# Kernel optimization log

Measured on AMD Instinct MI355X. Metric: run time of the kernel, lower is better.

## Reference

```python
import jax, jax.numpy as jnp
import numpy as np

N_NODES = 50000
N_EDGES = 800000
B, S, D = 512, 200, 128
H = 8


def setup_inputs() -> dict:
    key = jax.random.key(0)
    ks = iter(jax.random.split(key, 64))
    def nrm(shape, scale=0.05):
        return jax.random.normal(next(ks), shape, dtype=jnp.float32) * scale
    inp = {
        'hist_seq': jax.random.randint(next(ks), (B, S), 0, N_NODES, dtype=jnp.int32),
        'hist_answers': jax.random.randint(next(ks), (B, S), 0, 2, dtype=jnp.int32),
        'new_seq': jax.random.randint(next(ks), (B, S), 0, N_NODES, dtype=jnp.int32),
        'edge_index': jax.random.randint(next(ks), (2, N_EDGES), 0, N_NODES, dtype=jnp.int32),
        'node_x': nrm((N_NODES, D)),
        'gcn_w0': nrm((D, D)), 'gcn_b0': jnp.zeros((D,), jnp.float32),
        'gcn_w1': nrm((D, D)), 'gcn_b1': jnp.zeros((D,), jnp.float32),
        'gcn_w2': nrm((D, D)), 'gcn_b2': jnp.zeros((D,), jnp.float32),
        'ln0_g': jnp.ones((D,), jnp.float32), 'ln0_b': jnp.zeros((D,), jnp.float32),
        'ln1_g': jnp.ones((D,), jnp.float32), 'ln1_b': jnp.zeros((D,), jnp.float32),
        'ln2_g': jnp.ones((D,), jnp.float32), 'ln2_b': jnp.zeros((D,), jnp.float32),
        'ln3_g': jnp.ones((D,), jnp.float32), 'ln3_b': jnp.zeros((D,), jnp.float32),
        'corr_emb': nrm((2, D)),
        'lin0_w': nrm((2 * D, D)), 'lin0_b': jnp.zeros((D,), jnp.float32),
        'lin1_w': nrm((D, D)), 'lin2_w': nrm((D, D)), 'lin3_w': nrm((D, D)),
        'lin4_w': nrm((D, 1)), 'lin4_b': jnp.zeros((1,), jnp.float32),
        'pos_emb': nrm((S, D)),
        'mha_wq': nrm((D, D)), 'mha_bq': jnp.zeros((D,), jnp.float32),
        'mha_wk': nrm((D, D)), 'mha_bk': jnp.zeros((D,), jnp.float32),
        'mha_wv': nrm((D, D)), 'mha_bv': jnp.zeros((D,), jnp.float32),
        'mha_wo': nrm((D, D)), 'mha_bo': jnp.zeros((D,), jnp.float32),
        'ffn0_w': nrm((D, D)), 'ffn0_b': jnp.zeros((D,), jnp.float32),
        'ffn1_w': nrm((D, D)), 'ffn1_b': jnp.zeros((D,), jnp.float32),
    }
    return inp


def _layer_norm(x, g, b, eps=1e-5):
    m = jnp.mean(x, axis=-1, keepdims=True)
    v = jnp.var(x, axis=-1, keepdims=True)
    return (x - m) * jax.lax.rsqrt(v + eps) * g + b


def _forward(hist_seq, hist_answers, new_seq, edge_index, node_x,
             gcn_w0, gcn_b0, gcn_w1, gcn_b1, gcn_w2, gcn_b2,
             ln0_g, ln0_b, ln1_g, ln1_b, ln2_g, ln2_b, ln3_g, ln3_b,
             corr_emb, lin0_w, lin0_b, lin1_w, lin2_w, lin3_w, lin4_w, lin4_b,
             pos_emb, mha_wq, mha_bq, mha_wk, mha_bk, mha_wv, mha_bv,
             mha_wo, mha_bo, ffn0_w, ffn0_b, ffn1_w, ffn1_b):
    N = node_x.shape[0]
    loop = jnp.arange(N, dtype=edge_index.dtype)
    src = jnp.concatenate([edge_index[0], loop])  # self-loops as in PyG GCNConv
    dst = jnp.concatenate([edge_index[1], loop])
    deg = jax.ops.segment_sum(jnp.ones_like(dst, dtype=node_x.dtype), dst, num_segments=N)
    dis = jax.lax.rsqrt(deg)  # deg >= 1 (self-loops)
    norm = dis[src] * dis[dst]

    def gcn(x, W, b):
        xw = x @ W
        return jax.ops.segment_sum(norm[:, None] * xw[src], dst, num_segments=N) + b

    x = _layer_norm(jax.nn.relu(gcn(node_x, gcn_w0, gcn_b0)), ln0_g, ln0_b)
    x = _layer_norm(jax.nn.relu(gcn(x, gcn_w1, gcn_b1)), ln1_g, ln1_b)
    x = jax.nn.relu(gcn(x, gcn_w2, gcn_b2))  # last GCN layer: no LN

    # vectorized embedding gathers (the original's per-element loops)
    hist_emb = x[hist_seq]            # [B,S,D]
    new_emb = x[new_seq]              # [B,S,D]
    ans_emb = corr_emb[hist_answers]  # [B,S,D]

    inter = jnp.concatenate([hist_emb, ans_emb], axis=-1) @ lin0_w + lin0_b
    inter = inter + pos_emb[None]  # [B,S,D]

    v = inter @ lin1_w
    k = inter @ lin2_w
    q = new_emb @ lin3_w

    b_, s_, d_ = q.shape
    dh = d_ // H
    qh = (q @ mha_wq + mha_bq).reshape(b_, s_, H, dh)
    kh = (k @ mha_wk + mha_bk).reshape(b_, s_, H, dh)
    vh = (v @ mha_wv + mha_bv).reshape(b_, s_, H, dh)
    scores = jnp.einsum('bqhd,bkhd->bhqk', qh, kh) / jnp.sqrt(jnp.asarray(dh, q.dtype))
    causal = jnp.triu(jnp.ones((s_, s_), dtype=bool), k=1)
    scores = jnp.where(causal[None, None], -jnp.inf, scores)
    attn = jax.nn.softmax(scores, axis=-1)
    ao = jnp.einsum('bhqk,bkhd->bqhd', attn, vh).reshape(b_, s_, d_)
    ao = ao @ mha_wo + mha_bo

    atn = _layer_norm(ao + q, ln2_g, ln2_b)
    ffn = jax.nn.relu(atn @ ffn0_w + ffn0_b) @ ffn1_w + ffn1_b
    out = _layer_norm(ffn + atn, ln3_g, ln3_b)
    pred = (out @ lin4_w + lin4_b)[..., 0]  # squeeze -> [B,S]
    return pred


def reference(hist_seq, hist_answers, new_seq, edge_index, node_x,
              gcn_w0, gcn_b0, gcn_w1, gcn_b1, gcn_w2, gcn_b2,
              ln0_g, ln0_b, ln1_g, ln1_b, ln2_g, ln2_b, ln3_g, ln3_b,
              corr_emb, lin0_w, lin0_b, lin1_w, lin2_w, lin3_w, lin4_w, lin4_b,
              pos_emb, mha_wq, mha_bq, mha_wk, mha_bk, mha_wv, mha_bv,
              mha_wo, mha_bo, ffn0_w, ffn0_b, ffn1_w, ffn1_b):
    return _forward(hist_seq, hist_answers, new_seq, edge_index, node_x,
                    gcn_w0, gcn_b0, gcn_w1, gcn_b1, gcn_w2, gcn_b2,
                    ln0_g, ln0_b, ln1_g, ln1_b, ln2_g, ln2_b, ln3_g, ln3_b,
                    corr_emb, lin0_w, lin0_b, lin1_w, lin2_w, lin3_w, lin4_w, lin4_b,
                    pos_emb, mha_wq, mha_bq, mha_wk, mha_bk, mha_wv, mha_bv,
                    mha_wo, mha_bo, ffn0_w, ffn0_b, ffn1_w, ffn1_b)
```

## Files before the change

### kernel.cpp

```cpp
#include <hip/hip_runtime.h>
#include <math.h>

#define N_NODES 50000
#define N_EDGES 800000
#define B_ 512
#define S_ 200
#define D_ 128
#define BS_ (B_*S_)
#define PSTR 228

typedef unsigned short u16;
typedef unsigned int u32;
using bfrag = __attribute__((ext_vector_type(8))) short;
using f32x4 = __attribute__((ext_vector_type(4))) float;

__device__ __forceinline__ u16 f2bf(float f) {
  return (u16)((__float_as_uint(f) + 0x8000u) >> 16);
}
__device__ __forceinline__ float bf2f(u16 v) { return __uint_as_float(((u32)v) << 16); }
__device__ __forceinline__ float bflo(u32 v) { return __uint_as_float(v << 16); }
__device__ __forceinline__ float bfhi(u32 v) { return __uint_as_float(v & 0xffff0000u); }
__device__ __forceinline__ u32 pack2(float a, float b) {
  return (u32)f2bf(a) | ((u32)f2bf(b) << 16);
}
#define MFMA16(a, b, c) __builtin_amdgcn_mfma_f32_16x16x32_bf16((a), (b), (c), 0, 0, 0)

#define STAGE_W(Wsrc) \
  for (int i_ = threadIdx.x; i_ < 2048; i_ += 256) { \
    int c_ = i_ >> 4, kg_ = i_ & 15; \
    *(uint4*)(sW + c_ * 136 + kg_ * 8) = *(const uint4*)((Wsrc) + c_ * 128 + kg_ * 8); \
  }

__global__ void zero_i32_kernel(int* __restrict__ p, int n) {
  int i = blockIdx.x * 256 + threadIdx.x;
  if (i < n) p[i] = 0;
}

__global__ void f2bf8_kernel(const float* __restrict__ in, u16* __restrict__ out, int n8) {
  int i = blockIdx.x * 256 + threadIdx.x;
  if (i >= n8) return;
  float4 a = ((const float4*)in)[i * 2];
  float4 b = ((const float4*)in)[i * 2 + 1];
  uint4 o;
  o.x = pack2(a.x, a.y); o.y = pack2(a.z, a.w);
  o.z = pack2(b.x, b.y); o.w = pack2(b.z, b.w);
  ((uint4*)out)[i] = o;
}

__global__ __launch_bounds__(256) void wprep_kernel(
    const float* __restrict__ gcn_w0, const float* __restrict__ gcn_w1,
    const float* __restrict__ gcn_w2, const float* __restrict__ lin0_w,
    const float* __restrict__ lin3_w, const float* __restrict__ mha_wo,
    const float* __restrict__ ffn0_w, const float* __restrict__ ffn1_w,
    const float* __restrict__ lin1_w, const float* __restrict__ lin2_w,
    const float* __restrict__ mha_wq, const float* __restrict__ mha_wk,
    const float* __restrict__ mha_wv, const float* __restrict__ corr_emb,
    u16* __restrict__ g0T, u16* __restrict__ g1T, u16* __restrict__ g2T,
    u16* __restrict__ l0T, u16* __restrict__ l3T, u16* __restrict__ woT,
    u16* __restrict__ f0T, u16* __restrict__ f1T,
    u16* __restrict__ wqT, u16* __restrict__ wkT, u16* __restrict__ wvT,
    float* __restrict__ c01) {
  int bb = blockIdx.x;
  if (bb < 512) {
    const float* W; u16* D;
    switch (bb >> 6) {
      case 0: W = gcn_w0; D = g0T; break;
      case 1: W = gcn_w1; D = g1T; break;
      case 2: W = gcn_w2; D = g2T; break;
      case 3: W = lin0_w; D = l0T; break;
      case 4: W = lin3_w; D = l3T; break;
      case 5: W = mha_wo; D = woT; break;
      case 6: W = ffn0_w; D = f0T; break;
      default: W = ffn1_w; D = f1T; break;
    }
    int i = (bb & 63) * 256 + threadIdx.x;
    int k = i >> 7, c = i & 127;
    D[c * 128 + k] = f2bf(W[k * 128 + c]);
  } else if (bb < 704) {
    const float* X; const float* Y; u16* D;
    switch ((bb - 512) >> 6) {
      case 0: X = lin3_w; Y = mha_wq; D = wqT; break;
      case 1: X = lin2_w; Y = mha_wk; D = wkT; break;
      default: X = lin1_w; Y = mha_wv; D = wvT; break;
    }
    int i = ((bb - 512) & 63) * 256 + threadIdx.x;
    int k = i >> 7, c = i & 127;
    float acc = 0.f;
    for (int t = 0; t < 128; ++t) acc += X[k * 128 + t] * Y[t * 128 + c];
    D[c * 128 + k] = f2bf(acc);
  } else {
    int idx = threadIdx.x;
    int i = idx >> 7, j = idx & 127;
    float acc = 0.f;
    for (int t = 0; t < 128; ++t)
      acc += corr_emb[i * 128 + t] * lin0_w[128 * 128 + t * 128 + j];
    c01[idx] = acc;
  }
}

__global__ void pc_kernel(const float* __restrict__ lin0_b, const float* __restrict__ pos_emb,
                          const float* __restrict__ c01, float* __restrict__ pc) {
  int i = blockIdx.x * 256 + threadIdx.x;
  int c = i & 127, s = (i >> 7) % S_, a = i / (128 * S_);
  pc[i] = lin0_b[c] + pos_emb[s * 128 + c] + c01[a * 128 + c];
}

__global__ void hist_kernel(const int* __restrict__ dst, int* __restrict__ cnt, int E) {
  int e = blockIdx.x * 256 + threadIdx.x;
  if (e < E) atomicAdd(&cnt[dst[e]], 1);
}

__global__ __launch_bounds__(1024) void scanA_kernel(
    const int* __restrict__ cnt, int* __restrict__ locpref,
    int* __restrict__ btot, float* __restrict__ dis, int N) {
  __shared__ int wsum[16];
  int t = threadIdx.x, lane = t & 63, wid = t >> 6;
  int i = blockIdx.x * 1024 + t;
  int v = (i < N) ? cnt[i] : 0;
  if (i < N) dis[i] = rsqrtf(1.f + (float)v);
  int x = v;
  #pragma unroll
  for (int off = 1; off < 64; off <<= 1) {
    int y = __shfl_up(x, off);
    if (lane >= off) x += y;
  }
  if (lane == 63) wsum[wid] = x;
  __syncthreads();
  if (wid == 0 && lane < 16) {
    int s = wsum[lane];
    #pragma unroll
    for (int off = 1; off < 16; off <<= 1) {
      int y = __shfl_up(s, off);
      if (lane >= off) s += y;
    }
    wsum[lane] = s;
  }
  __syncthreads();
  int woff = (wid > 0) ? wsum[wid - 1] : 0;
  if (i < N) locpref[i] = woff + x - v;
  if (t == 1023) btot[blockIdx.x] = woff + x;
}

__global__ void scanB_kernel(const int* __restrict__ btot, int* __restrict__ boff, int nb) {
  int lane = threadIdx.x;
  int v = (lane < nb) ? btot[lane] : 0;
  int x = v;
  #pragma unroll
  for (int off = 1; off < 64; off <<= 1) {
    int y = __shfl_up(x, off);
    if (lane >= off) x += y;
  }
  if (lane < nb) boff[lane] = x - v;
}

__global__ void scanC_kernel(const int* __restrict__ locpref, const int* __restrict__ boff,
                             int* __restrict__ row_ptr, int* __restrict__ fill, int N) {
  int i = blockIdx.x * 256 + threadIdx.x;
  if (i < N) {
    int r = locpref[i] + boff[i >> 10];
    row_ptr[i] = r; fill[i] = r;
  }
  if (i == 0) row_ptr[N] = N_EDGES;
}

__global__ void scatter_kernel(const int* __restrict__ src, const int* __restrict__ dst,
                               int* __restrict__ fill, int* __restrict__ csr_src, int E) {
  int e = blockIdx.x * 256 + threadIdx.x;
  if (e >= E) return;
  int d = dst[e];
  int pos = atomicAdd(&fill[d], 1);
  csr_src[pos] = src[e];
}

__global__ __launch_bounds__(256) void gemm_bf16_kernel(
    const u16* __restrict__ A, const u16* __restrict__ wT,
    u16* __restrict__ C, int M) {
  __shared__ u16 ldsb[4][16 * 136];
  int t = threadIdx.x;
  int w = t >> 6, l = t & 63, lr = l & 15, lg = l >> 4;
  int r0 = blockIdx.x * 64 + w * 16;

  int row = r0 + lr;
  const u16* Arow = A + (size_t)(row < M ? row : 0) * 128;

  bfrag a[4];
  #pragma unroll
  for (int ks = 0; ks < 4; ++ks) a[ks] = *(const bfrag*)(Arow + ks * 32 + lg * 8);

  f32x4 acc[8];
  #pragma unroll
  for (int ct = 0; ct < 8; ++ct) acc[ct] = (f32x4){0.f, 0.f, 0.f, 0.f};
  #pragma unroll
  for (int ks = 0; ks < 4; ++ks)
    #pragma unroll
    for (int ct = 0; ct < 8; ++ct) {
      bfrag b = *(const bfrag*)(wT + (size_t)(ct * 16 + lr) * 128 + ks * 32 + lg * 8);
      acc[ct] = MFMA16(a[ks], b, acc[ct]);
    }
  #pragma unroll
  for (int ct = 0; ct < 8; ++ct)
    #pragma unroll
    for (int i = 0; i < 4; ++i)
      ldsb[w][(lg * 4 + i) * 136 + ct * 16 + lr] = f2bf(acc[ct][i]);
  #pragma unroll
  for (int j = 0; j < 4; ++j) {
    int c = j * 64 + l;
    int rw = c >> 4, ch = c & 15;
    int r = r0 + rw;
    if (r < M)
      *(uint4*)(C + (size_t)r * 128 + ch * 8) = *(const uint4*)&ldsb[w][rw * 136 + ch * 8];
  }
}

__global__ __launch_bounds__(256) void agg_kernel(
    const u16* __restrict__ xw, const float* __restrict__ dis,
    const int* __restrict__ row_ptr, const int* __restrict__ csr_src,
    const float* __restrict__ bias, const float* __restrict__ lng,
    const float* __restrict__ lnb, u16* __restrict__ out, int N, int doLN) {
  int t = threadIdx.x;
  int n = blockIdx.x * 4 + (t >> 6);
  if (n >= N) return;
  int l = t & 63, cg = l & 15, eg = l >> 4;
  float dn = dis[n];
  float acc[8] = {0.f, 0.f, 0.f, 0.f, 0.f, 0.f, 0.f, 0.f};
  if (eg == 0) {
    uint4 r = *(const uint4*)(xw + (size_t)n * 128 + cg * 8);
    float w = dn * dn;
    acc[0] += w * bflo(r.x); acc[1] += w * bfhi(r.x);
    acc[2] += w * bflo(r.y); acc[3] += w * bfhi(r.y);
    acc[4] += w * bflo(r.z); acc[5] += w * bfhi(r.z);
    acc[6] += w * bflo(r.w); acc[7] += w * bfhi(r.w);
  }
  int e1 = row_ptr[n + 1];
  int e = row_ptr[n] + eg;
  int sn = (e < e1) ? csr_src[e] : -1;
  while (sn >= 0) {
    int s = sn;
    e += 4;
    sn = (e < e1) ? csr_src[e] : -1;
    float w = dis[s] * dn;
    uint4 r = *(const uint4*)(xw + (size_t)s * 128 + cg * 8);
    acc[0] += w * bflo(r.x); acc[1] += w * bfhi(r.x);
    acc[2] += w * bflo(r.y); acc[3] += w * bfhi(r.y);
    acc[4] += w * bflo(r.z); acc[5] += w * bfhi(r.z);
    acc[6] += w * bflo(r.w); acc[7] += w * bfhi(r.w);
  }
  #pragma unroll
  for (int j = 0; j < 8; ++j) {
    acc[j] += __shfl_xor(acc[j], 16);
    acc[j] += __shfl_xor(acc[j], 32);
  }
  int c0 = cg * 8;
  #pragma unroll
  for (int j = 0; j < 8; ++j) acc[j] = fmaxf(acc[j] + bias[c0 + j], 0.f);
  if (doLN) {
    float s1 = 0.f, s2 = 0.f;
    #pragma unroll
    for (int j = 0; j < 8; ++j) { s1 += acc[j]; s2 += acc[j] * acc[j]; }
    #pragma unroll
    for (int off = 1; off < 16; off <<= 1) {
      s1 += __shfl_xor(s1, off);
      s2 += __shfl_xor(s2, off);
    }
    float mean = s1 * (1.f / 128.f);
    float var = s2 * (1.f / 128.f) - mean * mean;
    float inv = rsqrtf(var + 1e-5f);
    #pragma unroll
    for (int j = 0; j < 8; ++j)
      acc[j] = (acc[j] - mean) * inv * lng[c0 + j] + lnb[c0 + j];
  }
  if (eg == 0) {
    uint4 o;
    o.x = pack2(acc[0], acc[1]); o.y = pack2(acc[2], acc[3]);
    o.z = pack2(acc[4], acc[5]); o.w = pack2(acc[6], acc[7]);
    *(uint4*)(out + (size_t)n * 128 + cg * 8) = o;
  }
}

__global__ __launch_bounds__(256) void qkv_kernel(
    const u16* __restrict__ xa, const int* __restrict__ hist,
    const int* __restrict__ ans, const int* __restrict__ nseq,
    const u16* __restrict__ l0T, const float* __restrict__ pc,
    const u16* __restrict__ wkT, const float* __restrict__ bk,
    const u16* __restrict__ wvT, const float* __restrict__ bv,
    const u16* __restrict__ wqT, const float* __restrict__ bq,
    u16* __restrict__ khout, u16* __restrict__ vhout,
    u16* __restrict__ qhout, int nblk) {
  __shared__ u16 sW[128 * 136];
  __shared__ u16 ldsb[4][16 * 136];
  int bb = blockIdx.x;
  int t = threadIdx.x, w = t >> 6, l = t & 63, lr = l & 15, lg = l >> 4;
  f32x4 acc[8];

  if (bb < nblk) {
    int r0 = bb * 64 + w * 16;
    int arow = hist[r0 + lr];
    const u16* Arow = xa + (size_t)arow * 128;
    bfrag a[4];
    #pragma unroll
    for (int ks = 0; ks < 4; ++ks) a[ks] = *(const bfrag*)(Arow + ks * 32 + lg * 8);

    STAGE_W(l0T);
    __syncthreads();
    #pragma unroll
    for (int ct = 0; ct < 8; ++ct) acc[ct] = (f32x4){0.f, 0.f, 0.f, 0.f};
    #pragma unroll
    for (int ks = 0; ks < 4; ++ks)
      #pragma unroll
      for (int ct = 0; ct < 8; ++ct) {
        bfrag b = *(const bfrag*)(sW + (ct * 16 + lr) * 136 + ks * 32 + lg * 8);
        acc[ct] = MFMA16(a[ks], b, acc[ct]);
      }
    int pcoff[4];
    #pragma unroll
    for (int i = 0; i < 4; ++i) {
      int r = r0 + lg * 4 + i;
      pcoff[i] = (ans[r] * S_ + (r % S_)) * 128;
    }
    #pragma unroll
    for (int ct = 0; ct < 8; ++ct) {
      int col = ct * 16 + lr;
      #pragma unroll
      for (int i = 0; i < 4; ++i)
        ldsb[w][(lg * 4 + i) * 136 + col] = f2bf(acc[ct][i] + pc[pcoff[i] + col]);
    }
    bfrag a2[4];
    #pragma unroll
    for (int ks = 0; ks < 4; ++ks)
      a2[ks] = *(const bfrag*)(&ldsb[w][lr * 136 + ks * 32 + lg * 8]);
    __syncthreads();

    STAGE_W(wkT);
    __syncthreads();
    #pragma unroll
    for (int ct = 0; ct < 8; ++ct) acc[ct] = (f32x4){0.f, 0.f, 0.f, 0.f};
    #pragma unroll
    for (int ks = 0; ks < 4; ++ks)
      #pragma unroll
      for (int ct = 0; ct < 8; ++ct) {
        bfrag b = *(const bfrag*)(sW + (ct * 16 + lr) * 136 + ks * 32 + lg * 8);
        acc[ct] = MFMA16(a2[ks], b, acc[ct]);
      }
    #pragma unroll
    for (int ct = 0; ct < 8; ++ct)
      #pragma unroll
      for (int i = 0; i < 4; ++i)
        ldsb[w][(lg * 4 + i) * 136 + ct * 16 + lr] = f2bf(acc[ct][i] + bk[ct * 16 + lr]);
    #pragma unroll
    for (int j = 0; j < 4; ++j) {
      int c = j * 64 + l;
      int head = c >> 5, rw = (c >> 1) & 15, half = c & 1;
      *(uint4*)(khout + ((size_t)head * BS_ + r0 + rw) * 16 + half * 8) =
          *(const uint4*)&ldsb[w][rw * 136 + head * 16 + half * 8];
    }
    __syncthreads();

    STAGE_W(wvT);
    __syncthreads();
    #pragma unroll
    for (int ct = 0; ct < 8; ++ct) acc[ct] = (f32x4){0.f, 0.f, 0.f, 0.f};
    #pragma unroll
    for (int ks = 0; ks < 4; ++ks)
      #pragma unroll
      for (int ct = 0; ct < 8; ++ct) {
        bfrag b = *(const bfrag*)(sW + (ct * 16 + lr) * 136 + ks * 32 + lg * 8);
        acc[ct] = MFMA16(a2[ks], b, acc[ct]);
      }
    #pragma unroll
    for (int ct = 0; ct < 8; ++ct)
      #pragma unroll
      for (int i = 0; i < 4; ++i)
        ldsb[w][(lg * 4 + i) * 136 + ct * 16 + lr] = f2bf(acc[ct][i] + bv[ct * 16 + lr]);
    #pragma unroll
    for (int j = 0; j < 4; ++j) {
      int c = j * 64 + l;
      int head = c >> 5, rw = (c >> 1) & 15, half = c & 1;
      *(uint4*)(vhout + ((size_t)head * BS_ + r0 + rw) * 16 + half * 8) =
          *(const uint4*)&ldsb[w][rw * 136 + head * 16 + half * 8];
    }
  } else {
    int r0 = (bb - nblk) * 64 + w * 16;
    int arow = nseq[r0 + lr];
    const u16* Arow = xa + (size_t)arow * 128;
    bfrag a[4];
    #pragma unroll
    for (int ks = 0; ks < 4; ++ks) a[ks] = *(const bfrag*)(Arow + ks * 32 + lg * 8);

    STAGE_W(wqT);
    __syncthreads();
    #pragma unroll
    for (int ct = 0; ct < 8; ++ct) acc[ct] = (f32x4){0.f, 0.f, 0.f, 0.f};
    #pragma unroll
    for (int ks = 0; ks < 4; ++ks)
      #pragma unroll
      for (int ct = 0; ct < 8; ++ct) {
        bfrag b = *(const bfrag*)(sW + (ct * 16 + lr) * 136 + ks * 32 + lg * 8);
        acc[ct] = MFMA16(a[ks], b, acc[ct]);
      }
    #pragma unroll
    for (int ct = 0; ct < 8; ++ct)
      #pragma unroll
      for (int i = 0; i < 4; ++i)
        ldsb[w][(lg * 4 + i) * 136 + ct * 16 + lr] =
            f2bf((acc[ct][i] + bq[ct * 16 + lr]) * 0.25f);
    #pragma unroll
    for (int j = 0; j < 4; ++j) {
      int c = j * 64 + l;
      int head = c >> 5, rw = (c >> 1) & 15, half = c & 1;
      *(uint4*)(qhout + ((size_t)head * BS_ + r0 + rw) * 16 + half * 8) =
          *(const uint4*)&ldsb[w][rw * 136 + head * 16 + half * 8];
    }
  }
}

__global__ __launch_bounds__(256) void attn_mfma_kernel(
    u16* qh_ao, const u16* __restrict__ kh, const u16* __restrict__ vh) {
  __shared__ u16 Kl[208 * 24];
  __shared__ u16 Vt[16 * 232];
  __shared__ u16 Pl[4 * 16 * PSTR];
  int b = blockIdx.x >> 3, h = blockIdx.x & 7;
  int t = threadIdx.x;
  size_t base = ((size_t)h * BS_ + (size_t)b * S_) * 16;

  for (int i = t; i < 208 * 2; i += 256) {
    int key = i >> 1, d = (i & 1) * 8;
    uint4 v = make_uint4(0, 0, 0, 0);
    if (key < S_) v = *(const uint4*)(kh + base + (size_t)key * 16 + d);
    *(uint4*)(Kl + key * 24 + d) = v;
  }
  for (int i = t; i < 16 * 232; i += 256) {
    int d = i / 232, key = i - d * 232;
    Vt[d * 232 + key] = (key < S_) ? vh[base + (size_t)key * 16 + d] : (u16)0;
  }
  for (int i = t; i < 4 * 16 * PSTR / 2; i += 256) ((u32*)Pl)[i] = 0;
  __syncthreads();

  int w = t >> 6, l = t & 63, lr = l & 15, lg = l >> 4;
  u16* Pw = Pl + w * 16 * PSTR;
  const f32x4 zero4 = {0.f, 0.f, 0.f, 0.f};
  u32 qpack = (w == 0) ? 0xFC71u : (w == 1) ? 0xFB80u : (w == 2) ? 0xFA92u : 0x6543u;
  int qlocal = lg * 4;

  for (int s = 0; s < 4; ++s) {
    int qi = (qpack >> (4 * s)) & 15;
    if (qi == 15) break;
    bfrag aq = (bfrag){0, 0, 0, 0, 0, 0, 0, 0};
    int qrow = qi * 16 + lr;
    if (lg < 2 && qrow < S_)
      aq = *(const bfrag*)(qh_ao + base + (size_t)qrow * 16 + lg * 8);
    float rsum[4] = {0.f, 0.f, 0.f, 0.f};
    for (int kj = 0; kj < qi; ++kj) {
      bfrag bk = (bfrag){0, 0, 0, 0, 0, 0, 0, 0};
      if (lg < 2) bk = *(const bfrag*)(Kl + (kj * 16 + lr) * 24 + lg * 8);
      f32x4 sc = MFMA16(aq, bk, zero4);
      #pragma unroll
      for (int i = 0; i < 4; ++i) {
        float p = __expf(sc[i]);
        rsum[i] += p;
        Pw[(qlocal + i) * PSTR + kj * 16 + lr] = f2bf(p);
      }
    }
    {
      bfrag bk = (bfrag){0, 0, 0, 0, 0, 0, 0, 0};
      if (lg < 2) bk = *(const bfrag*)(Kl + (qi * 16 + lr) * 24 + lg * 8);
      f32x4 sc = MFMA16(aq, bk, zero4);
      #pragma unroll
      for (int i = 0; i < 4; ++i) {
        if (lr <= qlocal + i) {
          float p = __expf(sc[i]);
          rsum[i] += p;
          Pw[(qlocal + i) * PSTR + qi * 16 + lr] = f2bf(p);
        }
      }
    }
    #pragma unroll
    for (int i = 0; i < 4; ++i) {
      rsum[i] += __shfl_xor(rsum[i], 1);
      rsum[i] += __shfl_xor(rsum[i], 2);
      rsum[i] += __shfl_xor(rsum[i], 4);
      rsum[i] += __shfl_xor(rsum[i], 8);
    }
    f32x4 o = zero4;
    int ktmax = (qi + 2) >> 1;
    for (int kt = 0; kt < ktmax; ++kt) {
      bfrag ap = *(const bfrag*)(Pw + lr * PSTR + kt * 32 + lg * 8);
      bfrag bv = *(const bfrag*)(Vt + lr * 232 + kt * 32 + lg * 8);
      o = MFMA16(ap, bv, o);
    }
    #pragma unroll
    for (int i = 0; i < 4; ++i) {
      int q = qi * 16 + qlocal + i;
      if (q < S_) qh_ao[base + (size_t)q * 16 + lr] = f2bf(o[i] / rsum[i]);
    }
  }
}

__global__ __launch_bounds__(256) void out_kernel(
    const u16* __restrict__ ao, const u16* __restrict__ xa,
    const int* __restrict__ nseq,
    const u16* __restrict__ woT, const float* __restrict__ bo,
    const u16* __restrict__ l3T,
    const float* __restrict__ g2, const float* __restrict__ b2,
    const u16* __restrict__ f0T, const float* __restrict__ b0f,
    const u16* __restrict__ f1T, const float* __restrict__ b1f,
    const float* __restrict__ g3, const float* __restrict__ b3,
    const float* __restrict__ w4, const float* __restrict__ b4,
    float* __restrict__ pred) {
  __shared__ u16 sW[128 * 136];
  __shared__ u16 ldsb[4][16 * 136];
  int t = threadIdx.x, w = t >> 6, l = t & 63, lr = l & 15, lg = l >> 4;
  int r0 = blockIdx.x * 64 + w * 16;

  bfrag a_ao[4], a_xa[4];
  #pragma unroll
  for (int ks = 0; ks < 4; ++ks) {
    int head = ks * 2 + (lg >> 1);
    int d0 = (lg & 1) * 8;
    a_ao[ks] = *(const bfrag*)(ao + ((size_t)head * BS_ + r0 + lr) * 16 + d0);
  }
  {
    int arow = nseq[r0 + lr];
    const u16* Arow = xa + (size_t)arow * 128;
    #pragma unroll
    for (int ks = 0; ks < 4; ++ks) a_xa[ks] = *(const bfrag*)(Arow + ks * 32 + lg * 8);
  }

  f32x4 acc[8];
  #pragma unroll
  for (int ct = 0; ct < 8; ++ct) acc[ct] = (f32x4){0.f, 0.f, 0.f, 0.f};

  STAGE_W(woT);
  __syncthreads();
  #pragma unroll
  for (int ks = 0; ks < 4; ++ks)
    #pragma unroll
    for (int ct = 0; ct < 8; ++ct) {
      bfrag b = *(const bfrag*)(sW + (ct * 16 + lr) * 136 + ks * 32 + lg * 8);
      acc[ct] = MFMA16(a_ao[ks], b, acc[ct]);
    }
  __syncthreads();

  STAGE_W(l3T);
  __syncthreads();
  #pragma unroll
  for (int ks = 0; ks < 4; ++ks)
    #pragma unroll
    for (int ct = 0; ct < 8; ++ct) {
      bfrag b = *(const bfrag*)(sW + (ct * 16 + lr) * 136 + ks * 32 + lg * 8);
      acc[ct] = MFMA16(a_xa[ks], b, acc[ct]);
    }
  __syncthreads();

  #pragma unroll
  for (int ct = 0; ct < 8; ++ct) {
    float bcol = bo[ct * 16 + lr];
    #pragma unroll
    for (int i = 0; i < 4; ++i) acc[ct][i] += bcol;
  }
  bfrag a2[4];
  {
    float s1[4] = {0, 0, 0, 0}, s2[4] = {0, 0, 0, 0};
    #pragma unroll
    for (int ct = 0; ct < 8; ++ct)
      #pragma unroll
      for (int i = 0; i < 4; ++i) {
        s1[i] += acc[ct][i];
        s2[i] += acc[ct][i] * acc[ct][i];
      }
    #pragma unroll
    for (int i = 0; i < 4; ++i) {
      s1[i] += __shfl_xor(s1[i], 1); s2[i] += __shfl_xor(s2[i], 1);
      s1[i] += __shfl_xor(s1[i], 2); s2[i] += __shfl_xor(s2[i], 2);
      s1[i] += __shfl_xor(s1[i], 4); s2[i] += __shfl_xor(s2[i], 4);
      s1[i] += __shfl_xor(s1[i], 8); s2[i] += __shfl_xor(s2[i], 8);
    }
    float mean[4], inv[4];
    #pragma unroll
    for (int i = 0; i < 4; ++i) {
      mean[i] = s1[i] * (1.f / 128.f);
      float var = s2[i] * (1.f / 128.f) - mean[i] * mean[i];
      inv[i] = rsqrtf(var + 1e-5f);
    }
    #pragma unroll
    for (int ct = 0; ct < 8; ++ct) {
      int col = ct * 16 + lr;
      float gc = g2[col], bc = b2[col];
      #pragma unroll
      for (int i = 0; i < 4; ++i) {
        acc[ct][i] = (acc[ct][i] - mean[i]) * inv[i] * gc + bc;
        ldsb[w][(lg * 4 + i) * 136 + col] = f2bf(acc[ct][i]);
      }
    }
    #pragma unroll
    for (int ks = 0; ks < 4; ++ks)
      a2[ks] = *(const bfrag*)(&ldsb[w][lr * 136 + ks * 32 + lg * 8]);
  }

  STAGE_W(f0T);
  __syncthreads();
  f32x4 acc2[8];
  #pragma unroll
  for (int ct = 0; ct < 8; ++ct) acc2[ct] = (f32x4){0.f, 0.f, 0.f, 0.f};
  #pragma unroll
  for (int ks = 0; ks < 4; ++ks)
    #pragma unroll
    for (int ct = 0; ct < 8; ++ct) {
      bfrag b = *(const bfrag*)(sW + (ct * 16 + lr) * 136 + ks * 32 + lg * 8);
      acc2[ct] = MFMA16(a2[ks], b, acc2[ct]);
    }
  #pragma unroll
  for (int ct = 0; ct < 8; ++ct) {
    int col = ct * 16 + lr;
    float bcol = b0f[col];
    #pragma unroll
    for (int i = 0; i < 4; ++i)
      ldsb[w][(lg * 4 + i) * 136 + col] = f2bf(fmaxf(acc2[ct][i] + bcol, 0.f));
  }
  #pragma unroll
  for (int ks = 0; ks < 4; ++ks)
    a2[ks] = *(const bfrag*)(&ldsb[w][lr * 136 + ks * 32 + lg * 8]);
  __syncthreads();

  STAGE_W(f1T);
  __syncthreads();
  #pragma unroll
  for (int ct = 0; ct < 8; ++ct) acc2[ct] = (f32x4){0.f, 0.f, 0.f, 0.f};
  #pragma unroll
  for (int ks = 0; ks < 4; ++ks)
    #pragma unroll
    for (int ct = 0; ct < 8; ++ct) {
      bfrag b = *(const bfrag*)(sW + (ct * 16 + lr) * 136 + ks * 32 + lg * 8);
      acc2[ct] = MFMA16(a2[ks], b, acc2[ct]);
    }
  #pragma unroll
  for (int ct = 0; ct < 8; ++ct) {
    int col = ct * 16 + lr;
    float bcol = b1f[col];
    #pragma unroll
    for (int i = 0; i < 4; ++i) acc2[ct][i] += bcol + acc[ct][i];
  }
  {
    float s1[4] = {0, 0, 0, 0}, s2[4] = {0, 0, 0, 0};
    #pragma unroll
    for (int ct = 0; ct < 8; ++ct)
      #pragma unroll
      for (int i = 0; i < 4; ++i) {
        s1[i] += acc2[ct][i];
        s2[i] += acc2[ct][i] * acc2[ct][i];
      }
    #pragma unroll
    for (int i = 0; i < 4; ++i) {
      s1[i] += __shfl_xor(s1[i], 1); s2[i] += __shfl_xor(s2[i], 1);
      s1[i] += __shfl_xor(s1[i], 2); s2[i] += __shfl_xor(s2[i], 2);
      s1[i] += __shfl_xor(s1[i], 4); s2[i] += __shfl_xor(s2[i], 4);
      s1[i] += __shfl_xor(s1[i], 8); s2[i] += __shfl_xor(s2[i], 8);
    }
    float p[4] = {0, 0, 0, 0};
    #pragma unroll
    for (int i = 0; i < 4; ++i) {
      float mean = s1[i] * (1.f / 128.f);
      float var = s2[i] * (1.f / 128.f) - mean * mean;
      float inv = rsqrtf(var + 1e-5f);
      #pragma unroll
      for (int ct = 0; ct < 8; ++ct) {
        int col = ct * 16 + lr;
        p[i] += ((acc2[ct][i] - mean) * inv * g3[col] + b3[col]) * w4[col];
      }
    }
    #pragma unroll
    for (int i = 0; i < 4; ++i) {
      p[i] += __shfl_xor(p[i], 1);
      p[i] += __shfl_xor(p[i], 2);
      p[i] += __shfl_xor(p[i], 4);
      p[i] += __shfl_xor(p[i], 8);
    }
    if (lr == 0) {
      float bias4 = b4[0];
      #pragma unroll
      for (int i = 0; i < 4; ++i) pred[r0 + lg * 4 + i] = p[i] + bias4;
    }
  }
}

extern "C" void kernel_launch(void* const* d_in, const int* in_sizes, int n_in,
                              void* d_out, int out_size, void* d_ws, size_t ws_size,
                              hipStream_t stream) {
  const int* hist_seq = (const int*)d_in[0];
  const int* hist_ans = (const int*)d_in[1];
  const int* new_seq = (const int*)d_in[2];
  const int* edge_index = (const int*)d_in[3];
  const float* node_x = (const float*)d_in[4];
  const float* gcn_w0 = (const float*)d_in[5];
  const float* gcn_b0 = (const float*)d_in[6];
  const float* gcn_w1 = (const float*)d_in[7];
  const float* gcn_b1 = (const float*)d_in[8];
  const float* gcn_w2 = (const float*)d_in[9];
  const float* gcn_b2 = (const float*)d_in[10];
  const float* ln0_g = (const float*)d_in[11];
  const float* ln0_b = (const float*)d_in[12];
  const float* ln1_g = (const float*)d_in[13];
  const float* ln1_b = (const float*)d_in[14];
  const float* ln2_g = (const float*)d_in[15];
  const float* ln2_b = (const float*)d_in[16];
  const float* ln3_g = (const float*)d_in[17];
  const float* ln3_b = (const float*)d_in[18];
  const float* corr_emb = (const float*)d_in[19];
  const float* lin0_w = (const float*)d_in[20];
  const float* lin0_b = (const float*)d_in[21];
  const float* lin1_w = (const float*)d_in[22];
  const float* lin2_w = (const float*)d_in[23];
  const float* lin3_w = (const float*)d_in[24];
  const float* lin4_w = (const float*)d_in[25];
  const float* lin4_b = (const float*)d_in[26];
  const float* pos_emb = (const float*)d_in[27];
  const float* mha_wq = (const float*)d_in[28];
  const float* mha_bq = (const float*)d_in[29];
  const float* mha_wk = (const float*)d_in[30];
  const float* mha_bk = (const float*)d_in[31];
  const float* mha_wv = (const float*)d_in[32];
  const float* mha_bv = (const float*)d_in[33];
  const float* mha_wo = (const float*)d_in[34];
  const float* mha_bo = (const float*)d_in[35];
  const float* ffn0_w = (const float*)d_in[36];
  const float* ffn0_b = (const float*)d_in[37];
  const float* ffn1_w = (const float*)d_in[38];
  const float* ffn1_b = (const float*)d_in[39];
  (void)in_sizes; (void)n_in; (void)out_size;

  char* ws = (char*)d_ws;
  size_t off = 0;
  auto alloc = [&](size_t bytes) -> void* {
    void* p = ws + off;
    off += (bytes + 255) & ~(size_t)255;
    return p;
  };
  int* cnt = (int*)alloc((size_t)N_NODES * 4);
  int* row_ptr = (int*)alloc((size_t)(N_NODES + 1) * 4);
  int* fill = (int*)alloc((size_t)N_NODES * 4);
  int* locpref = (int*)alloc((size_t)N_NODES * 4);
  int* btot = (int*)alloc(64 * 4);
  int* boff = (int*)alloc(64 * 4);
  float* dis = (float*)alloc((size_t)N_NODES * 4);
  int* csr_src = (int*)alloc((size_t)N_EDGES * 4);
  const size_t WB = 128 * 128 * 2;
  u16* g0T = (u16*)alloc(WB);
  u16* g1T = (u16*)alloc(WB);
  u16* g2T = (u16*)alloc(WB);
  u16* l0T = (u16*)alloc(WB);
  u16* l3T = (u16*)alloc(WB);
  u16* woT = (u16*)alloc(WB);
  u16* f0T = (u16*)alloc(WB);
  u16* f1T = (u16*)alloc(WB);
  u16* wqT = (u16*)alloc(WB);
  u16* wkT = (u16*)alloc(WB);
  u16* wvT = (u16*)alloc(WB);
  float* c01 = (float*)alloc(2 * 128 * 4);
  float* pc = (float*)alloc((size_t)2 * S_ * 128 * 4);
  u16* xa = (u16*)alloc((size_t)N_NODES * 128 * 2);
  const size_t CB = (size_t)BS_ * 128 * 2;
  size_t RB = off;
  u16* bufQ = (u16*)(ws + RB);
  u16* bufK = (u16*)(ws + RB + CB);
  u16* bufV = (u16*)(ws + RB + 2 * CB);
  u16* xb = bufQ;
  u16* xw = bufQ + (size_t)N_NODES * 128;
  size_t need = RB + 3 * CB;
  if (ws_size < need) return;

  int nb = (N_NODES + 1023) / 1024;
  zero_i32_kernel<<<(N_NODES + 255) / 256, 256, 0, stream>>>(cnt, N_NODES);
  hist_kernel<<<(N_EDGES + 255) / 256, 256, 0, stream>>>(edge_index + N_EDGES, cnt, N_EDGES);
  scanA_kernel<<<nb, 1024, 0, stream>>>(cnt, locpref, btot, dis, N_NODES);
  scanB_kernel<<<1, 64, 0, stream>>>(btot, boff, nb);
  scanC_kernel<<<(N_NODES + 255) / 256, 256, 0, stream>>>(locpref, boff, row_ptr, fill, N_NODES);
  scatter_kernel<<<(N_EDGES + 255) / 256, 256, 0, stream>>>(edge_index, edge_index + N_EDGES,
                                                            fill, csr_src, N_EDGES);
  wprep_kernel<<<705, 256, 0, stream>>>(gcn_w0, gcn_w1, gcn_w2, lin0_w, lin3_w, mha_wo,
                                        ffn0_w, ffn1_w, lin1_w, lin2_w, mha_wq, mha_wk,
                                        mha_wv, corr_emb, g0T, g1T, g2T, l0T, l3T, woT,
                                        f0T, f1T, wqT, wkT, wvT, c01);
  pc_kernel<<<(2 * S_ * 128 + 255) / 256, 256, 0, stream>>>(lin0_b, pos_emb, c01, pc);
  f2bf8_kernel<<<(N_NODES * 16 + 255) / 256, 256, 0, stream>>>(node_x, xb, N_NODES * 16);

  int gN = (N_NODES + 63) / 64;
  int aN = (N_NODES + 3) / 4;

  gemm_bf16_kernel<<<gN, 256, 0, stream>>>(xb, g0T, xw, N_NODES);
  agg_kernel<<<aN, 256, 0, stream>>>(xw, dis, row_ptr, csr_src, gcn_b0, ln0_g, ln0_b, xa, N_NODES, 1);
  gemm_bf16_kernel<<<gN, 256, 0, stream>>>(xa, g1T, xw, N_NODES);
  agg_kernel<<<aN, 256, 0, stream>>>(xw, dis, row_ptr, csr_src, gcn_b1, ln1_g, ln1_b, xa, N_NODES, 1);
  gemm_bf16_kernel<<<gN, 256, 0, stream>>>(xa, g2T, xw, N_NODES);
  agg_kernel<<<aN, 256, 0, stream>>>(xw, dis, row_ptr, csr_src, gcn_b2, nullptr, nullptr, xa, N_NODES, 0);

  int gT = BS_ / 64;
  qkv_kernel<<<2 * gT, 256, 0, stream>>>(xa, hist_seq, hist_ans, new_seq,
                                         l0T, pc, wkT, mha_bk, wvT, mha_bv,
                                         wqT, mha_bq, bufK, bufV, bufQ, gT);
  attn_mfma_kernel<<<B_ * 8, 256, 0, stream>>>(bufQ, bufK, bufV);
  out_kernel<<<gT, 256, 0, stream>>>(bufQ, xa, new_seq, woT, mha_bo, l3T,
                                     ln2_g, ln2_b, f0T, ffn0_b, f1T, ffn1_b,
                                     ln3_g, ln3_b, lin4_w, lin4_b, (float*)d_out);
}
```

Measured before the change: 447.1 us.

## Keep attention probabilities in registers via transposed MFMA and lane shuffles

The attention kernel now computes K·Q^T instead of Q·K^T, so each lane holds probabilities for one query column. The P tile is then re-laid out with cross-lane shuffles into the B operand of the P·V MFMA, which removes the per-wave shared-memory P buffer, its zeroing, and the LDS round trip. Row sums now need only two xor shuffles, and the output is written as packed 8-byte stores. The cost is extra shuffles and selects per key tile, plus a fused loop over pairs of key tiles.

```diff
diff --git a/kernel.cpp b/kernel.cpp
--- a/kernel.cpp
+++ b/kernel.cpp
@@ -7,12 +7,12 @@
 #define S_ 200
 #define D_ 128
 #define BS_ (B_*S_)
-#define PSTR 228
 
 typedef unsigned short u16;
 typedef unsigned int u32;
 using bfrag = __attribute__((ext_vector_type(8))) short;
 using f32x4 = __attribute__((ext_vector_type(4))) float;
+using i32x4 = __attribute__((ext_vector_type(4))) int;
 
 __device__ __forceinline__ u16 f2bf(float f) {
   return (u16)((__float_as_uint(f) + 0x8000u) >> 16);
@@ -417,7 +417,6 @@
     u16* qh_ao, const u16* __restrict__ kh, const u16* __restrict__ vh) {
   __shared__ u16 Kl[208 * 24];
   __shared__ u16 Vt[16 * 232];
-  __shared__ u16 Pl[4 * 16 * PSTR];
   int b = blockIdx.x >> 3, h = blockIdx.x & 7;
   int t = threadIdx.x;
   size_t base = ((size_t)h * BS_ + (size_t)b * S_) * 16;
@@ -432,65 +431,84 @@
     int d = i / 232, key = i - d * 232;
     Vt[d * 232 + key] = (key < S_) ? vh[base + (size_t)key * 16 + d] : (u16)0;
   }
-  for (int i = t; i < 4 * 16 * PSTR / 2; i += 256) ((u32*)Pl)[i] = 0;
   __syncthreads();
 
   int w = t >> 6, l = t & 63, lr = l & 15, lg = l >> 4;
-  u16* Pw = Pl + w * 16 * PSTR;
   const f32x4 zero4 = {0.f, 0.f, 0.f, 0.f};
+  const bfrag zerob = (bfrag){0, 0, 0, 0, 0, 0, 0, 0};
   u32 qpack = (w == 0) ? 0xFC71u : (w == 1) ? 0xFB80u : (w == 2) ? 0xFA92u : 0x6543u;
-  int qlocal = lg * 4;
+  int srcA = lr + ((lg & 1) << 5);
+  int srcB = srcA + 16;
+  bool hiTile = (lg >= 2);
 
   for (int s = 0; s < 4; ++s) {
     int qi = (qpack >> (4 * s)) & 15;
     if (qi == 15) break;
-    bfrag aq = (bfrag){0, 0, 0, 0, 0, 0, 0, 0};
     int qrow = qi * 16 + lr;
+    bfrag qf = zerob;
     if (lg < 2 && qrow < S_)
-      aq = *(const bfrag*)(qh_ao + base + (size_t)qrow * 16 + lg * 8);
-    float rsum[4] = {0.f, 0.f, 0.f, 0.f};
-    for (int kj = 0; kj < qi; ++kj) {
-      bfrag bk = (bfrag){0, 0, 0, 0, 0, 0, 0, 0};
-      if (lg < 2) bk = *(const bfrag*)(Kl + (kj * 16 + lr) * 24 + lg * 8);
-      f32x4 sc = MFMA16(aq, bk, zero4);
-      #pragma unroll
-      for (int i = 0; i < 4; ++i) {
-        float p = __expf(sc[i]);
-        rsum[i] += p;
-        Pw[(qlocal + i) * PSTR + kj * 16 + lr] = f2bf(p);
-      }
-    }
-    {
-      bfrag bk = (bfrag){0, 0, 0, 0, 0, 0, 0, 0};
-      if (lg < 2) bk = *(const bfrag*)(Kl + (qi * 16 + lr) * 24 + lg * 8);
-      f32x4 sc = MFMA16(aq, bk, zero4);
-      #pragma unroll
-      for (int i = 0; i < 4; ++i) {
-        if (lr <= qlocal + i) {
-          float p = __expf(sc[i]);
-          rsum[i] += p;
-          Pw[(qlocal + i) * PSTR + qi * 16 + lr] = f2bf(p);
-        }
-      }
-    }
-    #pragma unroll
-    for (int i = 0; i < 4; ++i) {
-      rsum[i] += __shfl_xor(rsum[i], 1);
-      rsum[i] += __shfl_xor(rsum[i], 2);
-      rsum[i] += __shfl_xor(rsum[i], 4);
-      rsum[i] += __shfl_xor(rsum[i], 8);
-    }
+      qf = *(const bfrag*)(qh_ao + base + (size_t)qrow * 16 + lg * 8);
+    float rsum = 0.f;
     f32x4 o = zero4;
     int ktmax = (qi + 2) >> 1;
     for (int kt = 0; kt < ktmax; ++kt) {
-      bfrag ap = *(const bfrag*)(Pw + lr * PSTR + kt * 32 + lg * 8);
-      bfrag bv = *(const bfrag*)(Vt + lr * 232 + kt * 32 + lg * 8);
-      o = MFMA16(ap, bv, o);
-    }
-    #pragma unroll
-    for (int i = 0; i < 4; ++i) {
-      int q = qi * 16 + qlocal + i;
-      if (q < S_) qh_ao[base + (size_t)q * 16 + lr] = f2bf(o[i] / rsum[i]);
+      int kj0 = kt * 2, kj1 = kt * 2 + 1;
+      u32 P0t0, P1t0, P0t1 = 0, P1t1 = 0;
+      {
+        bfrag kf = zerob;
+        if (lg < 2) kf = *(const bfrag*)(Kl + (kj0 * 16 + lr) * 24 + lg * 8);
+        f32x4 sc = MFMA16(kf, qf, zero4);
+        float p0, p1, p2, p3;
+        if (kj0 == qi) {
+          p0 = (lg * 4 + 0 <= lr) ? __expf(sc[0]) : 0.f;
+          p1 = (lg * 4 + 1 <= lr) ? __expf(sc[1]) : 0.f;
+          p2 = (lg * 4 + 2 <= lr) ? __expf(sc[2]) : 0.f;
+          p3 = (lg * 4 + 3 <= lr) ? __expf(sc[3]) : 0.f;
+        } else {
+          p0 = __expf(sc[0]); p1 = __expf(sc[1]);
+          p2 = __expf(sc[2]); p3 = __expf(sc[3]);
+        }
+        rsum += (p0 + p1) + (p2 + p3);
+        P0t0 = pack2(p0, p1); P1t0 = pack2(p2, p3);
+      }
+      if (kj1 <= qi) {
+        bfrag kf = zerob;
+        if (lg < 2) kf = *(const bfrag*)(Kl + (kj1 * 16 + lr) * 24 + lg * 8);
+        f32x4 sc = MFMA16(kf, qf, zero4);
+        float p0, p1, p2, p3;
+        if (kj1 == qi) {
+          p0 = (lg * 4 + 0 <= lr) ? __expf(sc[0]) : 0.f;
+          p1 = (lg * 4 + 1 <= lr) ? __expf(sc[1]) : 0.f;
+          p2 = (lg * 4 + 2 <= lr) ? __expf(sc[2]) : 0.f;
+          p3 = (lg * 4 + 3 <= lr) ? __expf(sc[3]) : 0.f;
+        } else {
+          p0 = __expf(sc[0]); p1 = __expf(sc[1]);
+          p2 = __expf(sc[2]); p3 = __expf(sc[3]);
+        }
+        rsum += (p0 + p1) + (p2 + p3);
+        P0t1 = pack2(p0, p1); P1t1 = pack2(p2, p3);
+      }
+      u32 x0 = __shfl(P0t0, srcA), x1 = __shfl(P1t0, srcA);
+      u32 x2 = __shfl(P0t0, srcB), x3 = __shfl(P1t0, srcB);
+      u32 y0 = __shfl(P0t1, srcA), y1 = __shfl(P1t1, srcA);
+      u32 y2 = __shfl(P0t1, srcB), y3 = __shfl(P1t1, srcB);
+      i32x4 pi;
+      pi[0] = (int)(hiTile ? y0 : x0);
+      pi[1] = (int)(hiTile ? y1 : x1);
+      pi[2] = (int)(hiTile ? y2 : x2);
+      pi[3] = (int)(hiTile ? y3 : x3);
+      bfrag pb = __builtin_bit_cast(bfrag, pi);
+      bfrag vf = *(const bfrag*)(Vt + lr * 232 + kt * 32 + lg * 8);
+      o = MFMA16(vf, pb, o);
+    }
+    rsum += __shfl_xor(rsum, 16);
+    rsum += __shfl_xor(rsum, 32);
+    if (qrow < S_) {
+      float inv = 1.f / rsum;
+      uint2 ov;
+      ov.x = pack2(o[0] * inv, o[1] * inv);
+      ov.y = pack2(o[2] * inv, o[3] * inv);
+      *(uint2*)(qh_ao + base + (size_t)qrow * 16 + lg * 4) = ov;
     }
   }
 }
```

New measurement: 417.3 us. -6.7%, faster.
